# Kernel tuning notes

Hardware: AMD Instinct MI355X
Metric: run time of the kernel (lower is better)

## Reference

```python
import jax, jax.numpy as jnp
import numpy as np

B, C, H, W = 4, 512, 32, 32
HEADS = 8
EPS = 1e-5


def setup_inputs() -> dict:
    key = jax.random.key(0)
    ks = jax.random.split(key, 9)
    s = 1.0 / np.sqrt(C)
    return {
        "x": jax.random.normal(ks[0], (B, C, H, W), dtype=jnp.float32),
        "w_q": jax.random.normal(ks[1], (C, C), dtype=jnp.float32) * s,  # Conv2d 1x1, no bias
        "w_k": jax.random.normal(ks[2], (C, C), dtype=jnp.float32) * s,
        "w_v": jax.random.normal(ks[3], (C, C), dtype=jnp.float32) * s,
        "w_head": jax.random.normal(ks[4], (HEADS, HEADS), dtype=jnp.float32) * (1.0 / np.sqrt(HEADS)),
        "in_gamma": jnp.ones((HEADS,), dtype=jnp.float32) + 0.1 * jax.random.normal(ks[5], (HEADS,), dtype=jnp.float32),
        "in_beta": 0.1 * jax.random.normal(ks[6], (HEADS,), dtype=jnp.float32),
        "w_proj": jax.random.normal(ks[7], (C, C), dtype=jnp.float32) * s,
        "b_proj": 0.02 * jax.random.normal(ks[8], (C,), dtype=jnp.float32),
    }


def reference(x, w_q, w_k, w_v, w_head, in_gamma, in_beta, w_proj, b_proj):
    b, c, h, w = x.shape
    heads = w_head.shape[0]
    hd = c // heads
    t = h * w
    scale = hd ** (-0.5)

    xf = x.reshape(b, c, t)  # [B,C,T]
    # 1x1 convs == channel matmuls
    q = jnp.einsum('oc,bct->bot', w_q, xf).reshape(b, heads, hd, t)
    k = jnp.einsum('oc,bct->bot', w_k, xf).reshape(b, heads, hd, t)
    v = jnp.einsum('oc,bct->bot', w_v, xf).reshape(b, heads, hd, t)

    attn = jnp.einsum('bhdq,bhdT->bhqT', q, k) * scale           # [B,heads,T,T]
    attn = jnp.einsum('gh,bhqT->bgqT', w_head, attn)             # head-mixing 1x1 conv
    attn = jax.nn.softmax(attn, axis=-1)
    # InstanceNorm2d over the (T,T) spatial dims, per head, biased variance
    mean = jnp.mean(attn, axis=(-2, -1), keepdims=True)
    var = jnp.var(attn, axis=(-2, -1), keepdims=True)
    attn = (attn - mean) / jnp.sqrt(var + EPS)
    attn = attn * in_gamma[None, :, None, None] + in_beta[None, :, None, None]

    out = jnp.einsum('bhqT,bhdT->bhqd', attn, v)                 # [B,heads,T,hd]
    out = out.reshape(b, t, c)                                   # same row-major flatten as torch .view
    out = out @ w_proj.T + b_proj                                # Linear
    return out.transpose(0, 2, 1).reshape(b, c, h, w)
```

## Files before the change

### kernel.cpp

```cpp
#include <hip/hip_runtime.h>
#include <hip/hip_bf16.h>

#define B_ 4
#define C_ 512
#define T_ 1024
#define SCALE_ 0.125f
#define EPS_ 1e-5f

typedef unsigned short u16;
typedef __attribute__((ext_vector_type(8))) unsigned short u16x8;
typedef __attribute__((ext_vector_type(4))) unsigned short u16x4;
typedef __attribute__((ext_vector_type(8))) short s16x8;
typedef __attribute__((ext_vector_type(4))) float f32x4;

#define QT_OFF    (0x0ull)
#define KS_OFF    (0x400000ull)
#define VS_OFF    (0x800000ull)
#define XT_OFF    (0xC00000ull)
#define WB_OFF    (0x1480000ull)
#define LP_OFF    (0x1680000ull)
#define L2P_OFF   (0x1700000ull)
#define WS_OFF    (0x1780000ull)
#define VSUM_OFF  (0x17A0000ull)
#define OP_OFF    (0x2000000ull)

static __device__ __forceinline__ u16 f2bf(float f) {
  unsigned u = __float_as_uint(f);
  unsigned r = (u + 0x7fff + ((u >> 16) & 1)) >> 16;
  return (u16)r;
}
static __device__ __forceinline__ float b2f(u16 x) {
  return __uint_as_float(((unsigned)x) << 16);
}
static __device__ __forceinline__ f32x4 mfma16(s16x8 a, s16x8 b, f32x4 c) {
  return __builtin_amdgcn_mfma_f32_16x16x32_bf16(a, b, c, 0, 0, 0);
}
#define BARSYNC()                                       \
  {                                                     \
    asm volatile("s_waitcnt lgkmcnt(0)" ::: "memory");  \
    __builtin_amdgcn_s_barrier();                       \
  }

__global__ __launch_bounds__(256) void prep_k(
    const float* __restrict__ x, const float* __restrict__ wq,
    const float* __restrict__ wk, const float* __restrict__ wv,
    const float* __restrict__ wp, u16* __restrict__ wb,
    float* __restrict__ ws, float* __restrict__ vsum, u16* __restrict__ xt) {
  const int id = blockIdx.x;
  const int tid = threadIdx.x;
  __shared__ float Ts[64][65];
  if (id < 512) {
    const int i = (id << 8) + tid;
    const int idx = i << 3;
    const int which = idx >> 18;
    const int off = idx & 262143;
    const float* s = which == 0 ? wq : which == 1 ? wk : which == 2 ? wv : wp;
    const float4 f0 = *(const float4*)(s + off);
    const float4 f1 = *(const float4*)(s + off + 4);
    u16x8 o;
    o[0] = f2bf(f0.x); o[1] = f2bf(f0.y); o[2] = f2bf(f0.z); o[3] = f2bf(f0.w);
    o[4] = f2bf(f1.x); o[5] = f2bf(f1.y); o[6] = f2bf(f1.z); o[7] = f2bf(f1.w);
    *(u16x8*)(wb + idx) = o;
  } else if (id < 640) {
    const int idx = ((id - 512) << 8) + tid;
    if (id - 512 < 8) vsum[idx] = 0.f;
    const int o = idx >> 6, d = idx & 63;
    float s = 0.f;
#pragma unroll
    for (int j = 0; j < 8; ++j) s += wp[(o << 9) + (j << 6) + d];
    ws[idx] = s;
  } else {
    const int id3 = id - 640;
    const int b = id3 >> 7, rem = id3 & 127;
    const int t0 = (rem & 15) << 6;
    const int c0 = (rem >> 4) << 6;
    const float* __restrict__ X = x + (size_t)b * (C_ * (size_t)T_);
    u16* __restrict__ Xt = xt + (size_t)b * (T_ * (size_t)C_);
#pragma unroll
    for (int i = 0; i < 4; ++i) {
      const int e = tid + (i << 8);
      const int r = e >> 4, c4 = e & 15;
      const float4 v =
          *(const float4*)(X + (size_t)(c0 + r) * T_ + t0 + (c4 << 2));
      Ts[r][(c4 << 2) + 0] = v.x; Ts[r][(c4 << 2) + 1] = v.y;
      Ts[r][(c4 << 2) + 2] = v.z; Ts[r][(c4 << 2) + 3] = v.w;
    }
    __syncthreads();
#pragma unroll
    for (int i = 0; i < 2; ++i) {
      const int e = tid + (i << 8);
      const int tt = e >> 3, c8 = e & 7;
      u16x8 o;
#pragma unroll
      for (int j = 0; j < 8; ++j) o[j] = f2bf(Ts[(c8 << 3) + j][tt]);
      *(u16x8*)(Xt + (size_t)(t0 + tt) * C_ + c0 + (c8 << 3)) = o;
    }
  }
}

__global__ __launch_bounds__(256) void gemm_qkv(
    const u16* __restrict__ xt, const u16* __restrict__ wqb,
    const u16* __restrict__ wkb, const u16* __restrict__ wvb,
    u16* __restrict__ qto, u16* __restrict__ ks, u16* __restrict__ vs,
    float* __restrict__ vsum) {
  const int z = blockIdx.z;
  const int tid = threadIdx.x;
  const int w = tid >> 6, lane = tid & 63, lr = lane & 15, lq = lane >> 4;
  const int wm = (w >> 1) << 6, wn = (w & 1) << 5;
  __shared__ __align__(16) u16 As[128][72];
  __shared__ __align__(16) u16 Bs[64][72];
  u16* Ts = &As[0][0];
  const u16 *Ag, *Bg;
  int m0, n0, mode, b;
  if (z < 8) {
    const int which = z >> 2;
    b = z & 3;
    Ag = xt + (size_t)b * (T_ * (size_t)C_);
    m0 = blockIdx.x << 7;
    Bg = which ? wkb : wqb;
    n0 = blockIdx.y << 6;
    mode = which;
  } else {
    b = z - 8;
    const int ti = (blockIdx.y << 3) | blockIdx.x;
    Ag = wvb;
    m0 = (ti >> 4) << 7;
    Bg = xt + (size_t)b * (T_ * (size_t)C_);
    n0 = (ti & 15) << 6;
    mode = 2;
  }
  u16x8 rA[4], rB[2];
#define LOADQ(K)                                                          \
  {                                                                       \
    _Pragma("unroll") for (int it = 0; it < 4; ++it) {                    \
      const int e = tid + (it << 8);                                      \
      const int r = e >> 3, c8 = (e & 7) << 3;                            \
      rA[it] = *(const u16x8*)(Ag + (size_t)(m0 + r) * C_ + (K) + c8);    \
    }                                                                     \
    _Pragma("unroll") for (int it = 0; it < 2; ++it) {                    \
      const int e = tid + (it << 8);                                      \
      const int r = e >> 3, c8 = (e & 7) << 3;                            \
      rB[it] = *(const u16x8*)(Bg + (size_t)(n0 + r) * C_ + (K) + c8);    \
    }                                                                     \
  }
  f32x4 acc[4][2] = {};
  LOADQ(0);
  for (int k0 = 0; k0 < C_; k0 += 64) {
    if (k0) BARSYNC();
#pragma unroll
    for (int it = 0; it < 4; ++it) {
      const int e = tid + (it << 8);
      *(u16x8*)&As[e >> 3][(e & 7) << 3] = rA[it];
    }
#pragma unroll
    for (int it = 0; it < 2; ++it) {
      const int e = tid + (it << 8);
      *(u16x8*)&Bs[e >> 3][(e & 7) << 3] = rB[it];
    }
    if (k0 < C_ - 64) LOADQ(k0 + 64);
    BARSYNC();
#pragma unroll
    for (int kf = 0; kf < 2; ++kf) {
      const int ko = (kf << 5) + (lq << 3);
      s16x8 a[4], bb[2];
#pragma unroll
      for (int i = 0; i < 4; ++i) a[i] = *(const s16x8*)&As[wm + (i << 4) + lr][ko];
#pragma unroll
      for (int j = 0; j < 2; ++j) bb[j] = *(const s16x8*)&Bs[wn + (j << 4) + lr][ko];
#pragma unroll
      for (int i = 0; i < 4; ++i)
#pragma unroll
        for (int j = 0; j < 2; ++j) acc[i][j] = mfma16(a[i], bb[j], acc[i][j]);
    }
  }
#undef LOADQ
  if (mode == 0) {
    u16* Y = qto + (size_t)b * (T_ * (size_t)C_);
#pragma unroll
    for (int i = 0; i < 4; ++i) {
      const int row = wm + (i << 4) + (lq << 2);
#pragma unroll
      for (int j = 0; j < 2; ++j) {
        const int col = wn + (j << 4) + lr;
#pragma unroll
        for (int r = 0; r < 4; ++r)
          Y[(size_t)(m0 + row + r) * C_ + n0 + col] =
              f2bf(acc[i][j][r] * SCALE_);
      }
    }
    return;
  }
  if (mode == 2) {
#pragma unroll
    for (int i = 0; i < 4; ++i)
#pragma unroll
      for (int r = 0; r < 4; ++r) {
        float s = acc[i][0][r] + acc[i][1][r];
        s += __shfl_xor(s, 1, 64);
        s += __shfl_xor(s, 2, 64);
        s += __shfl_xor(s, 4, 64);
        s += __shfl_xor(s, 8, 64);
        if (lr == 0) {
          const int o = m0 + wm + (i << 4) + (lq << 2) + r;
          atomicAdd(&vsum[(((b << 3) | (o >> 6)) << 6) | (o & 63)], s);
        }
      }
  }
  BARSYNC();
#pragma unroll
  for (int i = 0; i < 4; ++i)
#pragma unroll
    for (int j = 0; j < 2; ++j)
#pragma unroll
      for (int r = 0; r < 4; ++r)
        Ts[(wm + (i << 4) + (lq << 2) + r) * 72 + wn + (j << 4) + lr] =
            f2bf(acc[i][j][r]);
  __syncthreads();
  const int ch = tid >> 4, part = tid & 15;
  if (mode == 1) {
    const int t32l = ch >> 2, half = (ch >> 1) & 1, fl = ch & 1;
    const int t32g = (m0 >> 5) + t32l, fg = (n0 >> 5) + fl;
    u16* dst =
        ks + (((((size_t)((b << 5) | t32g) << 1) | half) << 4 | fg) << 9);
#pragma unroll
    for (int u = 0; u < 4; ++u) {
      const int lanek = (u << 4) + part;
      const int quadk = lanek >> 4, lrk = lanek & 15;
      const int rr = ((lrk >> 2) << 3) | (half << 2) | (lrk & 3);
      const u16x8 v =
          *(const u16x8*)&Ts[((t32l << 5) + rr) * 72 + (fl << 5) + (quadk << 3)];
      *(u16x8*)(dst + (lanek << 3)) = v;
    }
  } else {
    const int gl = ch >> 3, t32l = (ch >> 2) & 1, dj = ch & 3;
    const int gg = (m0 >> 6) + gl, t32g = (n0 >> 5) + t32l;
    u16* dst =
        vs + (((((size_t)((b << 3) | gg) << 5) | t32g) << 2 | dj) << 9);
#pragma unroll
    for (int u = 0; u < 4; ++u) {
      const int lanev = (u << 4) + part;
      const int quadv = lanev >> 4, lrv = lanev & 15;
      const u16x8 v = *(const u16x8*)&Ts[((gl << 6) + (dj << 4) + lrv) * 72 +
                                         (t32l << 5) + (quadv << 3)];
      *(u16x8*)(dst + (lanev << 3)) = v;
    }
  }
}

__global__ __launch_bounds__(512, 4) void attn_fused(
    const u16* __restrict__ Qt, const u16* __restrict__ KS,
    const u16* __restrict__ VS, const float* __restrict__ wh,
    float* __restrict__ Opart, float* __restrict__ lpart,
    float* __restrict__ l2part) {
  const int id = blockIdx.x;
  const int xcd = id & 7;
  const int b = xcd >> 1;
  const int hi = id >> 3;
  const int qb = ((xcd & 1) << 5) | (hi & 31);
  const int tq = hi >> 5;
  const int q0 = qb << 4;
  const int tid = threadIdx.x;
  const int w = tid >> 6, lane = tid & 63;
  const int lr = lane & 15, quad = lane >> 4;

  __shared__ __align__(16) u16 Qs[16][522];
  __shared__ __align__(16) u16 Plds[8][16][136];
  float* Sbuf = (float*)&Plds[0][0][0];

  {
    const u16* Qb = Qt + ((size_t)b * T_ + q0) * C_;
    for (int i = tid; i < 1024; i += 512) {
      const int r = i >> 6, c8 = i & 63;
      *(u16x8*)&Qs[r][c8 << 3] = *(const u16x8*)(Qb + (size_t)r * C_ + (c8 << 3));
    }
  }

  const u16* __restrict__ Qrow = &Qs[lr][quad << 3];
  const int g = w;
  const int win = w >> 1, half = w & 1;
  const int swz = lr & 7;
  const u16* __restrict__ Vc =
      VS + (((size_t)((b << 3) | g)) << 16) + (lane << 3);

  float lacc[8] = {}, l2acc[8] = {};
  f32x4 acc[4] = {};

  __syncthreads();

  for (int c = 0; c < 4; ++c) {
    const int t32k = (tq << 4) + (c << 2) + win;
    const u16* __restrict__ Kc =
        KS + (((size_t)((((b << 5) | t32k) << 1) | half)) << 13) + (lane << 3);
    f32x4 m[8] = {};
#pragma unroll 4
    for (int h = 0; h < 8; ++h) {
      f32x4 a0 = {0.f, 0.f, 0.f, 0.f};
      const s16x8 qf0 = *(const s16x8*)(Qrow + (h << 6));
      const s16x8 k0 = *(const s16x8*)(Kc + (h << 10));
      a0 = mfma16(k0, qf0, a0);
      const s16x8 qf1 = *(const s16x8*)(Qrow + (h << 6) + 32);
      const s16x8 k1 = *(const s16x8*)(Kc + (h << 10) + 512);
      a0 = mfma16(k1, qf1, a0);
#pragma unroll
      for (int gg = 0; gg < 8; ++gg) {
        const float wgh = wh[(gg << 3) + h];
        m[gg] += a0 * wgh;
      }
    }
    const int wgrp = ((win << 2) | quad) ^ swz;
#pragma unroll
    for (int gg = 0; gg < 8; ++gg) {
      f32x4 e0;
#pragma unroll
      for (int k = 0; k < 4; ++k) e0[k] = __expf(m[gg][k]);
      u16x4 o;
#pragma unroll
      for (int k = 0; k < 4; ++k) o[k] = f2bf(e0[k]);
      *(u16x4*)&Plds[gg][lr][(wgrp << 3) + (half << 2)] = o;
      lacc[gg] += e0[0] + e0[1] + e0[2] + e0[3];
      l2acc[gg] += e0[0] * e0[0] + e0[1] * e0[1] + e0[2] * e0[2] + e0[3] * e0[3];
    }
    __syncthreads();
#pragma unroll
    for (int tw = 0; tw < 4; ++tw) {
      const int t32v = (tq << 4) + (c << 2) + tw;
      const int rgrp = ((tw << 2) | quad) ^ swz;
      const s16x8 pa = *(const s16x8*)&Plds[g][lr][rgrp << 3];
#pragma unroll
      for (int dj = 0; dj < 4; ++dj) {
        const s16x8 vb =
            *(const s16x8*)(Vc + ((size_t)t32v << 11) + (dj << 9));
        acc[dj] = mfma16(pa, vb, acc[dj]);
      }
    }
    __syncthreads();
  }

  const int bg = (b << 3) + g;
  const size_t obase = ((((size_t)(tq << 5) + bg) << 10) + q0) * 64;
#pragma unroll
  for (int dj = 0; dj < 4; ++dj) {
    const int d = (dj << 4) + lr;
#pragma unroll
    for (int r = 0; r < 4; ++r) {
      const int q = (quad << 2) + r;
      Opart[obase + (size_t)q * 64 + d] = acc[dj][r];
    }
  }

  float* lbuf = Sbuf;
  float* l2buf = Sbuf + 1024;
#pragma unroll
  for (int gg = 0; gg < 8; ++gg) {
    float l = lacc[gg];
    l += __shfl_xor(l, 16, 64);
    l += __shfl_xor(l, 32, 64);
    float l2 = l2acc[gg];
    l2 += __shfl_xor(l2, 16, 64);
    l2 += __shfl_xor(l2, 32, 64);
    if (quad == 0) {
      lbuf[(w << 7) + (gg << 4) + lr] = l;
      l2buf[(w << 7) + (gg << 4) + lr] = l2;
    }
  }
  __syncthreads();
  if (lane < 16) {
    float l = 0.f, l2 = 0.f;
#pragma unroll
    for (int w2 = 0; w2 < 8; ++w2) {
      l += lbuf[(w2 << 7) + (g << 4) + lr];
      l2 += l2buf[(w2 << 7) + (g << 4) + lr];
    }
    const size_t li = (((size_t)(tq << 5) + bg) << 10) + q0 + lr;
    lpart[li] = l;
    l2part[li] = l2;
  }
}

__global__ __launch_bounds__(256) void gemm_proj(
    const float* __restrict__ Opart, const u16* __restrict__ wpb,
    const float* __restrict__ lpart, const float* __restrict__ l2part,
    const float* __restrict__ gamma, const float* __restrict__ beta,
    const float* __restrict__ ws, const float* __restrict__ bp,
    const float* __restrict__ vsum, float* __restrict__ y) {
  const int b = blockIdx.z;
  const int m0 = blockIdx.y << 6;
  const int n0 = blockIdx.x << 6;
  const int gidx = blockIdx.x >> 1;
  const int bg = (b << 3) + gidx;
  __shared__ __align__(16) u16 As[64][72];
  __shared__ __align__(16) u16 Bs[64][72];
  __shared__ float red[4];
  __shared__ float albc[2];
  __shared__ float b2s[64];
  __shared__ float linvS[512];
  const int tid = threadIdx.x;
  const int w = tid >> 6, lane = tid & 63, lr = lane & 15, lq = lane >> 4;
  const int mw = (w >> 1) << 5, nw = (w & 1) << 5;
  u16x8 rA[2];
  f32x4 rB[2][2][2];
#define LOADP(K)                                                            \
  {                                                                         \
    _Pragma("unroll") for (int it = 0; it < 2; ++it) {                      \
      const int e = tid + (it << 8);                                        \
      const int r = e >> 3, c8 = (e & 7) << 3;                              \
      rA[it] = *(const u16x8*)(wpb + (size_t)(m0 + r) * C_ + (K) + c8);     \
      const int q = (((n0 + r) & 127) << 3) + ((K) >> 6);                   \
      _Pragma("unroll") for (int tq = 0; tq < 2; ++tq) {                    \
        const float* src =                                                  \
            Opart + ((((size_t)((tq << 5) + bg)) << 10) + q) * 64 + c8;     \
        rB[it][tq][0] = *(const f32x4*)(src);                               \
        rB[it][tq][1] = *(const f32x4*)(src + 4);                           \
      }                                                                     \
    }                                                                       \
  }
  LOADP(0);
  {
    const size_t p0 = ((size_t)bg) << 10, p1 = ((size_t)(32 + bg)) << 10;
    const f32x4 la = *(const f32x4*)(lpart + p0 + (tid << 2));
    const f32x4 lb = *(const f32x4*)(lpart + p1 + (tid << 2));
    const f32x4 l2a = *(const f32x4*)(l2part + p0 + (tid << 2));
    const f32x4 l2b = *(const f32x4*)(l2part + p1 + (tid << 2));
    float ssq = 0.f;
#pragma unroll
    for (int k = 0; k < 4; ++k) {
      const float l = la[k] + lb[k];
      ssq += (l2a[k] + l2b[k]) / (l * l);
    }
#pragma unroll
    for (int off = 32; off; off >>= 1) ssq += __shfl_xor(ssq, off, 64);
    if (lane == 0) red[w] = ssq;
    const int qb0 = (n0 & 127) << 3;
#pragma unroll
    for (int j = 0; j < 2; ++j) {
      const int qq = (tid << 1) + j;
      const float l = lpart[p0 + qb0 + qq] + lpart[p1 + qb0 + qq];
      linvS[qq] = 1.f / l;
    }
  }
  __syncthreads();
  if (tid == 0) {
    const float s = red[0] + red[1] + red[2] + red[3];
    const float mean = 0.0009765625f;
    const float var = s * (1.f / 1048576.f) - mean * mean;
    const float al = gamma[gidx] * rsqrtf(var + EPS_);
    albc[0] = al;
    albc[1] = beta[gidx] - al * mean;
  }
  __syncthreads();
  if (tid < 64) {
    const int o = m0 + tid;
    const float* wr = ws + (o << 6);
    const float* vsr = vsum + (bg << 6);
    float acc = 0.f;
#pragma unroll
    for (int d = 0; d < 64; d += 4) {
      const float4 vv4 = *(const float4*)(vsr + d);
      const float4 ws4 = *(const float4*)(wr + d);
      acc += ws4.x * vv4.x + ws4.y * vv4.y + ws4.z * vv4.z + ws4.w * vv4.w;
    }
    b2s[tid] = bp[o] + albc[1] * acc;
  }
  f32x4 acc[2][2] = {};
  for (int k0 = 0; k0 < C_; k0 += 64) {
    if (k0) BARSYNC();
    __syncthreads();
#pragma unroll
    for (int it = 0; it < 2; ++it) {
      const int e = tid + (it << 8);
      const int r = e >> 3, c8 = (e & 7) << 3;
      *(u16x8*)&As[r][c8] = rA[it];
      const float li = linvS[(r << 3) + (k0 >> 6)];
      u16x8 o;
#pragma unroll
      for (int k = 0; k < 4; ++k) {
        o[k] = f2bf((rB[it][0][0][k] + rB[it][1][0][k]) * li);
        o[k + 4] = f2bf((rB[it][0][1][k] + rB[it][1][1][k]) * li);
      }
      *(u16x8*)&Bs[r][c8] = o;
    }
    if (k0 < C_ - 64) LOADP(k0 + 64);
    BARSYNC();
#pragma unroll
    for (int kf = 0; kf < 2; ++kf) {
      const int ko = (kf << 5) + (lq << 3);
      s16x8 a[2], bb[2];
#pragma unroll
      for (int i = 0; i < 2; ++i) a[i] = *(const s16x8*)&As[mw + (i << 4) + lr][ko];
#pragma unroll
      for (int j = 0; j < 2; ++j) bb[j] = *(const s16x8*)&Bs[nw + (j << 4) + lr][ko];
#pragma unroll
      for (int i = 0; i < 2; ++i)
#pragma unroll
        for (int j = 0; j < 2; ++j) acc[i][j] = mfma16(a[i], bb[j], acc[i][j]);
    }
  }
#undef LOADP
  const float al = albc[0];
#pragma unroll
  for (int i = 0; i < 2; ++i) {
    const int row = mw + (i << 4) + (lq << 2);
#pragma unroll
    for (int j = 0; j < 2; ++j) {
      const int col = nw + (j << 4) + lr;
#pragma unroll
      for (int r = 0; r < 4; ++r)
        y[(size_t)b * (C_ * (size_t)T_) + (size_t)(m0 + row + r) * T_ + n0 + col] =
            acc[i][j][r] * al + b2s[row + r];
    }
  }
}

extern "C" void kernel_launch(void* const* d_in, const int* in_sizes, int n_in,
                              void* d_out, int out_size, void* d_ws,
                              size_t ws_size, hipStream_t stream) {
  const float* x = (const float*)d_in[0];
  const float* wq = (const float*)d_in[1];
  const float* wk = (const float*)d_in[2];
  const float* wv = (const float*)d_in[3];
  const float* wh = (const float*)d_in[4];
  const float* gm = (const float*)d_in[5];
  const float* bt = (const float*)d_in[6];
  const float* wp = (const float*)d_in[7];
  const float* bp = (const float*)d_in[8];
  float* y = (float*)d_out;
  char* wsb = (char*)d_ws;

  u16* Qt = (u16*)(wsb + QT_OFF);
  u16* KS = (u16*)(wsb + KS_OFF);
  u16* VS = (u16*)(wsb + VS_OFF);
  u16* Xt = (u16*)(wsb + XT_OFF);
  float* vsum = (float*)(wsb + VSUM_OFF);
  u16* Wb = (u16*)(wsb + WB_OFF);
  u16* WQb = Wb;
  u16* WKb = Wb + 262144;
  u16* WVb = Wb + 524288;
  u16* WPb = Wb + 786432;
  float* lpart = (float*)(wsb + LP_OFF);
  float* l2part = (float*)(wsb + L2P_OFF);
  float* ws = (float*)(wsb + WS_OFF);
  float* Opart = (float*)(wsb + OP_OFF);

  prep_k<<<dim3(1152), 256, 0, stream>>>(x, wq, wk, wv, wp, Wb, ws, vsum, Xt);
  gemm_qkv<<<dim3(8, 8, 12), 256, 0, stream>>>(Xt, WQb, WKb, WVb, Qt, KS, VS,
                                               vsum);
  attn_fused<<<dim3(512), 512, 0, stream>>>(Qt, KS, VS, wh, Opart, lpart,
                                            l2part);
  gemm_proj<<<dim3(16, 8, 4), 256, 0, stream>>>(Opart, WPb, lpart, l2part, gm,
                                                bt, ws, bp, vsum, y);
}
```

Before: 150.1 us.

## Double-buffer QKV GEMM register prefetch and vectorize Q output stores

The QKV projection GEMM now holds two register stage sets and prefetches two K-slices ahead, so each global load has more MFMA work to hide behind. The loop is unrolled by two and adds an extra barrier per half-step. The Q output path now stages the scaled tile through LDS and writes 16-byte vector rows instead of scattered 2-byte stores. The attention kernel also drops the XOR swizzle on the P tile in LDS in favour of plain indexing, which removes some index math but may bring back bank conflicts.

```diff
diff --git a/kernel.cpp b/kernel.cpp
--- a/kernel.cpp
+++ b/kernel.cpp
@@ -129,67 +129,63 @@
     n0 = (ti & 15) << 6;
     mode = 2;
   }
-  u16x8 rA[4], rB[2];
-#define LOADQ(K)                                                          \
+  u16x8 rA0[4], rB0[2], rA1[4], rB1[2];
+#define LOADQ(RA, RB, K)                                                  \
   {                                                                       \
     _Pragma("unroll") for (int it = 0; it < 4; ++it) {                    \
       const int e = tid + (it << 8);                                      \
       const int r = e >> 3, c8 = (e & 7) << 3;                            \
-      rA[it] = *(const u16x8*)(Ag + (size_t)(m0 + r) * C_ + (K) + c8);    \
+      RA[it] = *(const u16x8*)(Ag + (size_t)(m0 + r) * C_ + (K) + c8);    \
     }                                                                     \
     _Pragma("unroll") for (int it = 0; it < 2; ++it) {                    \
       const int e = tid + (it << 8);                                      \
       const int r = e >> 3, c8 = (e & 7) << 3;                            \
-      rB[it] = *(const u16x8*)(Bg + (size_t)(n0 + r) * C_ + (K) + c8);    \
+      RB[it] = *(const u16x8*)(Bg + (size_t)(n0 + r) * C_ + (K) + c8);    \
     }                                                                     \
   }
+#define WRITEQ(RA, RB)                                       \
+  {                                                          \
+    _Pragma("unroll") for (int it = 0; it < 4; ++it) {       \
+      const int e = tid + (it << 8);                         \
+      *(u16x8*)&As[e >> 3][(e & 7) << 3] = RA[it];           \
+    }                                                        \
+    _Pragma("unroll") for (int it = 0; it < 2; ++it) {       \
+      const int e = tid + (it << 8);                         \
+      *(u16x8*)&Bs[e >> 3][(e & 7) << 3] = RB[it];           \
+    }                                                        \
+  }
+#define MFMAQ()                                                                \
+  {                                                                            \
+    _Pragma("unroll") for (int kf = 0; kf < 2; ++kf) {                         \
+      const int ko = (kf << 5) + (lq << 3);                                    \
+      s16x8 a[4], bb[2];                                                       \
+      _Pragma("unroll") for (int i = 0; i < 4; ++i) a[i] =                     \
+          *(const s16x8*)&As[wm + (i << 4) + lr][ko];                          \
+      _Pragma("unroll") for (int j = 0; j < 2; ++j) bb[j] =                    \
+          *(const s16x8*)&Bs[wn + (j << 4) + lr][ko];                          \
+      _Pragma("unroll") for (int i = 0; i < 4; ++i)                            \
+          _Pragma("unroll") for (int j = 0; j < 2; ++j) acc[i][j] =            \
+              mfma16(a[i], bb[j], acc[i][j]);                                  \
+    }                                                                          \
+  }
   f32x4 acc[4][2] = {};
-  LOADQ(0);
-  for (int k0 = 0; k0 < C_; k0 += 64) {
+  LOADQ(rA0, rB0, 0);
+  LOADQ(rA1, rB1, 64);
+  for (int k0 = 0; k0 < C_; k0 += 128) {
     if (k0) BARSYNC();
-#pragma unroll
-    for (int it = 0; it < 4; ++it) {
-      const int e = tid + (it << 8);
-      *(u16x8*)&As[e >> 3][(e & 7) << 3] = rA[it];
-    }
-#pragma unroll
-    for (int it = 0; it < 2; ++it) {
-      const int e = tid + (it << 8);
-      *(u16x8*)&Bs[e >> 3][(e & 7) << 3] = rB[it];
-    }
-    if (k0 < C_ - 64) LOADQ(k0 + 64);
+    WRITEQ(rA0, rB0);
+    if (k0 + 128 < C_) LOADQ(rA0, rB0, k0 + 128);
     BARSYNC();
-#pragma unroll
-    for (int kf = 0; kf < 2; ++kf) {
-      const int ko = (kf << 5) + (lq << 3);
-      s16x8 a[4], bb[2];
-#pragma unroll
-      for (int i = 0; i < 4; ++i) a[i] = *(const s16x8*)&As[wm + (i << 4) + lr][ko];
-#pragma unroll
-      for (int j = 0; j < 2; ++j) bb[j] = *(const s16x8*)&Bs[wn + (j << 4) + lr][ko];
-#pragma unroll
-      for (int i = 0; i < 4; ++i)
-#pragma unroll
-        for (int j = 0; j < 2; ++j) acc[i][j] = mfma16(a[i], bb[j], acc[i][j]);
-    }
+    MFMAQ();
+    BARSYNC();
+    WRITEQ(rA1, rB1);
+    if (k0 + 192 < C_) LOADQ(rA1, rB1, k0 + 192);
+    BARSYNC();
+    MFMAQ();
   }
 #undef LOADQ
-  if (mode == 0) {
-    u16* Y = qto + (size_t)b * (T_ * (size_t)C_);
-#pragma unroll
-    for (int i = 0; i < 4; ++i) {
-      const int row = wm + (i << 4) + (lq << 2);
-#pragma unroll
-      for (int j = 0; j < 2; ++j) {
-        const int col = wn + (j << 4) + lr;
-#pragma unroll
-        for (int r = 0; r < 4; ++r)
-          Y[(size_t)(m0 + row + r) * C_ + n0 + col] =
-              f2bf(acc[i][j][r] * SCALE_);
-      }
-    }
-    return;
-  }
+#undef WRITEQ
+#undef MFMAQ
   if (mode == 2) {
 #pragma unroll
     for (int i = 0; i < 4; ++i)
@@ -207,6 +203,7 @@
       }
   }
   BARSYNC();
+  const float osc = (mode == 0) ? SCALE_ : 1.0f;
 #pragma unroll
   for (int i = 0; i < 4; ++i)
 #pragma unroll
@@ -214,8 +211,18 @@
 #pragma unroll
       for (int r = 0; r < 4; ++r)
         Ts[(wm + (i << 4) + (lq << 2) + r) * 72 + wn + (j << 4) + lr] =
-            f2bf(acc[i][j][r]);
+            f2bf(acc[i][j][r] * osc);
   __syncthreads();
+  if (mode == 0) {
+    u16* Y = qto + (size_t)b * (T_ * (size_t)C_);
+    const int row = tid >> 1, ch32 = (tid & 1) << 5;
+    u16* dst = Y + (size_t)(m0 + row) * C_ + n0 + ch32;
+    const u16* src = &Ts[row * 72 + ch32];
+#pragma unroll
+    for (int u = 0; u < 4; ++u)
+      *(u16x8*)(dst + (u << 3)) = *(const u16x8*)(src + (u << 3));
+    return;
+  }
   const int ch = tid >> 4, part = tid & 15;
   if (mode == 1) {
     const int t32l = ch >> 2, half = (ch >> 1) & 1, fl = ch & 1;
@@ -278,7 +285,6 @@
   const u16* __restrict__ Qrow = &Qs[lr][quad << 3];
   const int g = w;
   const int win = w >> 1, half = w & 1;
-  const int swz = lr & 7;
   const u16* __restrict__ Vc =
       VS + (((size_t)((b << 3) | g)) << 16) + (lane << 3);
 
@@ -307,7 +313,6 @@
         m[gg] += a0 * wgh;
       }
     }
-    const int wgrp = ((win << 2) | quad) ^ swz;
 #pragma unroll
     for (int gg = 0; gg < 8; ++gg) {
       f32x4 e0;
@@ -316,7 +321,7 @@
       u16x4 o;
 #pragma unroll
       for (int k = 0; k < 4; ++k) o[k] = f2bf(e0[k]);
-      *(u16x4*)&Plds[gg][lr][(wgrp << 3) + (half << 2)] = o;
+      *(u16x4*)&Plds[gg][lr][(win << 5) + (quad << 3) + (half << 2)] = o;
       lacc[gg] += e0[0] + e0[1] + e0[2] + e0[3];
       l2acc[gg] += e0[0] * e0[0] + e0[1] * e0[1] + e0[2] * e0[2] + e0[3] * e0[3];
     }
@@ -324,8 +329,7 @@
 #pragma unroll
     for (int tw = 0; tw < 4; ++tw) {
       const int t32v = (tq << 4) + (c << 2) + tw;
-      const int rgrp = ((tw << 2) | quad) ^ swz;
-      const s16x8 pa = *(const s16x8*)&Plds[g][lr][rgrp << 3];
+      const s16x8 pa = *(const s16x8*)&Plds[g][lr][(tw << 5) + (quad << 3)];
 #pragma unroll
       for (int dj = 0; dj < 4; ++dj) {
         const s16x8 vb =
```

Result: faster. 146.3 us (-2.6%).
